# Kernel optimization log

Measured on AMD Instinct MI355X. Metric: run time of the kernel, lower is better.

The kernel has to match this reference:

```python
import jax, jax.numpy as jnp
import numpy as np

B, N, C = 32, 1024, 768
H = 12
HD = C // H            # 64
M = 2 * HD             # rand_feat_dim = head_dim * rand_feat_dim_ratio(2) = 128
LAM = 0.1
NUM_STEP = 8
EPS = 1e-12


def setup_inputs() -> dict:
    key = jax.random.key(0)
    ks = jax.random.split(key, 4)
    x = jax.random.normal(ks[0], (B, N, C), dtype=jnp.float32)
    qkv_w = jax.random.normal(ks[1], (2 * C, C), dtype=jnp.float32) * 0.02
    proj_w = jax.random.normal(ks[2], (C, C), dtype=jnp.float32) * 0.02
    proj_b = jnp.zeros((C,), dtype=jnp.float32)
    rand_matrix = jax.random.normal(ks[3], (H, HD, M), dtype=jnp.float32)
    learned_k = jnp.eye(M, dtype=jnp.float32)
    learned_lam = jnp.ones((1,), dtype=jnp.float32)
    learned_L = jnp.ones((1,), dtype=jnp.float32)
    return {"x": x, "qkv_w": qkv_w, "proj_w": proj_w, "proj_b": proj_b,
            "rand_matrix": rand_matrix, "learned_k": learned_k,
            "learned_lam": learned_lam, "learned_L": learned_L}


def _soft(z, thresh):
    # sign(z) * GELU(|z| - thresh), exact (erf) GELU as in torch nn.GELU()
    return jnp.sign(z) * jax.nn.gelu(jnp.abs(z) - thresh, approximate=False)


def reference(x, qkv_w, proj_w, proj_b, rand_matrix, learned_k, learned_lam, learned_L):
    scale = HD ** -0.5
    qkv = (x @ qkv_w.T).reshape(B, N, 2, H, HD).transpose(2, 0, 3, 1, 4)  # [2,B,H,N,HD]
    q, v = qkv[0], qkv[1]
    q = q * (scale ** 0.5)
    # performer-style positive random features: exp(x @ proj - ||x||^2/2)/sqrt(m)
    qf = jnp.exp(jnp.einsum('bhnd,hdm->bhnm', q, rand_matrix)
                 - jnp.sum(q * q, axis=-1, keepdims=True) / 2) / (M ** 0.5)
    # F.normalize(p=2, dim=-2): normalize each feature column over tokens
    qf = qf / jnp.maximum(jnp.linalg.norm(qf, axis=-2, keepdims=True), EPS)
    kk = jnp.einsum('bhnm,bhnp->bhmp', qf, qf)        # [B,H,M,M]
    inp = jnp.einsum('bhnm,bhnd->bhmd', qf, v)        # [B,H,M,HD]
    # ISTA-like sparse reconstruction
    L = jax.lax.stop_gradient(jnp.max(jnp.sum(jnp.abs(kk), axis=-1), axis=-1))[..., None, None] + 1.0
    lam_learned = learned_lam * LAM                    # broadcastable scalar
    Ll = L / learned_L                                 # [B,H,1,1]
    kk_l = jnp.einsum('mp,bhpq,qr->bhmr', learned_k, kk, learned_k)
    xs = _soft(inp, lam_learned)
    for _ in range(NUM_STEP):
        xs = xs - (jnp.einsum('bhmp,bhpd->bhmd', kk_l, xs) - inp) / Ll
        xs = _soft(xs, lam_learned / Ll)
    out = jnp.einsum('bhnm,bhmd->bhnd', qf, xs)        # [B,H,N,HD]
    out = out.transpose(0, 2, 1, 3).reshape(B, N, C)
    return out @ proj_w.T + proj_b
```

## Files before the change

kernel.cpp:

```cpp
#include <hip/hip_runtime.h>
#include <math.h>

typedef unsigned short u16;
typedef unsigned int u32;
typedef _Float16 f16;
typedef __attribute__((ext_vector_type(8))) short bf16x8;
typedef __attribute__((ext_vector_type(8))) _Float16 f16x8;
typedef __attribute__((ext_vector_type(4))) float f32x4;

constexpr int Bc = 32, Nc = 1024, Cc = 768, Hc = 12, HDc = 64, Mc = 128;
constexpr int NUM_STEP_C = 8;
constexpr float QSCALE = 0.35355339059327376f;
constexpr float INV_SQRT_M = 0.088388347648318447f;
constexpr float EPSC = 1e-12f;
constexpr int FS = 136;

__device__ __forceinline__ float softf(float z, float thr) {
  float az = fabsf(z) - thr;
  float g = 0.5f * az * (1.0f + erff(az * 0.70710678118654752f));
  return (z > 0.f) ? g : ((z < 0.f) ? -g : 0.f);
}

__device__ __forceinline__ u16 f2bf(float f) {
  u32 u = __float_as_uint(f);
  u += 0x7fffu + ((u >> 16) & 1u);
  return (u16)(u >> 16);
}

__device__ __forceinline__ f32x4 fzero() {
  f32x4 z; z[0] = 0.f; z[1] = 0.f; z[2] = 0.f; z[3] = 0.f; return z;
}

__device__ __forceinline__ f32x4 mfma16(bf16x8 a, bf16x8 b, f32x4 c) {
  return __builtin_amdgcn_mfma_f32_16x16x32_bf16(a, b, c, 0, 0, 0);
}
__device__ __forceinline__ f32x4 mfma16h(f16x8 a, f16x8 b, f32x4 c) {
  return __builtin_amdgcn_mfma_f32_16x16x32_f16(a, b, c, 0, 0, 0);
}

#define SWZ_COL(col, row) ((col) ^ (((row) & 7) << 3))

__device__ __forceinline__ void stage_swz(const u16* __restrict__ g, int ld,
                                          u16* lds, int w, int lane) {
  const int rr = lane >> 3;
  const int cs = ((lane & 7) ^ rr) << 3;
#pragma unroll
  for (int c = 0; c < 4; ++c) {
    const int r0 = w * 32 + c * 8;
    __builtin_amdgcn_global_load_lds(
        (const __attribute__((address_space(1))) void*)(g + (size_t)(r0 + rr) * ld + cs),
        (__attribute__((address_space(3))) void*)(lds + r0 * 64), 16, 0, 0);
  }
}

__global__ __launch_bounds__(256) void prep_kernel(
    const float* __restrict__ x, const float* __restrict__ qw,
    const float* __restrict__ pw, const float* __restrict__ rnd,
    const float* __restrict__ lkf, u16* __restrict__ xbf,
    u16* __restrict__ wbf, u16* __restrict__ pwbf, u16* __restrict__ randt,
    f16* __restrict__ lk16, f16* __restrict__ lkT16) {
  const int NX8 = 3145728, NW8 = 147456, NP8 = 73728, NR = 98304;
  const int NK8 = 2048, NKT = 16384;
  const int total = NX8 + NW8 + NP8 + NR + NK8 + NKT;
  for (int idx = blockIdx.x * 256 + threadIdx.x; idx < total;
       idx += gridDim.x * 256) {
    if (idx < NX8 + NW8 + NP8) {
      const float* src; u16* dst; int k;
      if (idx < NX8) { src = x; dst = xbf; k = idx; }
      else if (idx < NX8 + NW8) { src = qw; dst = wbf; k = idx - NX8; }
      else { src = pw; dst = pwbf; k = idx - NX8 - NW8; }
      float4 a = *(const float4*)(src + (size_t)k * 8);
      float4 b = *(const float4*)(src + (size_t)k * 8 + 4);
      uint4 o;
      o.x = (u32)f2bf(a.x) | ((u32)f2bf(a.y) << 16);
      o.y = (u32)f2bf(a.z) | ((u32)f2bf(a.w) << 16);
      o.z = (u32)f2bf(b.x) | ((u32)f2bf(b.y) << 16);
      o.w = (u32)f2bf(b.z) | ((u32)f2bf(b.w) << 16);
      *(uint4*)(dst + (size_t)k * 8) = o;
    } else if (idx < NX8 + NW8 + NP8 + NR) {
      int k = idx - NX8 - NW8 - NP8;
      int h = k >> 13, rem = k & 8191, m = rem >> 6, d = rem & 63;
      randt[k] = f2bf(rnd[(size_t)h * 8192 + d * 128 + m]);
    } else if (idx < NX8 + NW8 + NP8 + NR + NK8) {
      int k = idx - (NX8 + NW8 + NP8 + NR);
      float4 a = *(const float4*)(lkf + (size_t)k * 8);
      float4 b = *(const float4*)(lkf + (size_t)k * 8 + 4);
      union { f16 h[8]; uint4 u; } z;
      z.h[0] = (f16)a.x; z.h[1] = (f16)a.y; z.h[2] = (f16)a.z; z.h[3] = (f16)a.w;
      z.h[4] = (f16)b.x; z.h[5] = (f16)b.y; z.h[6] = (f16)b.z; z.h[7] = (f16)b.w;
      *(uint4*)(lk16 + (size_t)k * 8) = z.u;
    } else {
      int k = idx - (NX8 + NW8 + NP8 + NR + NK8);
      int c = k >> 7, p = k & 127;
      lkT16[k] = (f16)lkf[p * 128 + c];
    }
  }
}

__global__ __launch_bounds__(256) void qkv_qf_kernel(
    const u16* __restrict__ xbf, const u16* __restrict__ wbf,
    const u16* __restrict__ randt, u16* __restrict__ qft,
    u16* __restrict__ vbt) {
  __shared__ __align__(16) u16 SH[32768];
  const int t = threadIdx.x;
  const int hblk = blockIdx.x;
  const int lin = (hblk & 7) * 384 + (hblk >> 3);
  const int bi = lin / 12, bj = lin % 12;
  const int w = t >> 6, lane = t & 63, ln = lane & 15, kg = lane >> 4;
  const int wr = w >> 1, wc = w & 1;
  f32x4 acc[4][4];
#pragma unroll
  for (int i = 0; i < 4; ++i)
#pragma unroll
    for (int j = 0; j < 4; ++j) acc[i][j] = fzero();
  const u16* Ag = xbf + (size_t)(bi * 128) * Cc;
  const u16* Bg = wbf + (size_t)(bj * 128) * Cc;
  stage_swz(Ag, Cc, SH, w, lane);
  stage_swz(Bg, Cc, SH + 8192, w, lane);
  __syncthreads();
  int cur = 0;
  for (int tt = 0; tt < 12; ++tt) {
    if (tt < 11) {
      stage_swz(Ag + (tt + 1) * 64, Cc, SH + (cur ^ 1) * 16384, w, lane);
      stage_swz(Bg + (tt + 1) * 64, Cc, SH + 8192 + (cur ^ 1) * 16384, w, lane);
    }
    const u16* Als = SH + cur * 16384;
    const u16* Bls = SH + 8192 + cur * 16384;
#pragma unroll
    for (int ks = 0; ks < 2; ++ks) {
      const int cb = ks * 32 + kg * 8;
      bf16x8 af[4], bf[4];
#pragma unroll
      for (int i = 0; i < 4; ++i)
        af[i] = *(const bf16x8*)(Als + (wr * 64 + i * 16 + ln) * 64 +
                                 SWZ_COL(cb, ln));
#pragma unroll
      for (int j = 0; j < 4; ++j)
        bf[j] = *(const bf16x8*)(Bls + (wc * 64 + j * 16 + ln) * 64 +
                                 SWZ_COL(cb, ln));
#pragma unroll
      for (int i = 0; i < 4; ++i)
#pragma unroll
        for (int j = 0; j < 4; ++j) acc[i][j] = mfma16(af[i], bf[j], acc[i][j]);
    }
    __syncthreads();
    cur ^= 1;
  }
  const int b = bi >> 3;
  const int ntile = (bi & 7) * 128;
  if (bj >= 6) {
    const int h = (bj - 6) * 2 + wc;
    u16* vt = vbt + ((size_t)(b * Hc + h) * 64) * 1024;
#pragma unroll
    for (int i = 0; i < 4; ++i)
#pragma unroll
      for (int j = 0; j < 4; ++j) {
        int d = j * 16 + ln;
        int n0 = ntile + wr * 64 + i * 16 + kg * 4;
        uint2 pv;
        pv.x = (u32)f2bf(acc[i][j][0]) | ((u32)f2bf(acc[i][j][1]) << 16);
        pv.y = (u32)f2bf(acc[i][j][2]) | ((u32)f2bf(acc[i][j][3]) << 16);
        *(uint2*)(vt + (size_t)d * 1024 + n0) = pv;
      }
  } else {
#pragma unroll
    for (int i = 0; i < 4; ++i)
#pragma unroll
      for (int j = 0; j < 4; ++j) acc[i][j] *= QSCALE;
    float hn[4][4];
#pragma unroll
    for (int i = 0; i < 4; ++i)
#pragma unroll
      for (int r = 0; r < 4; ++r) {
        float s = acc[i][0][r] * acc[i][0][r] + acc[i][1][r] * acc[i][1][r] +
                  acc[i][2][r] * acc[i][2][r] + acc[i][3][r] * acc[i][3][r];
        s += __shfl_xor(s, 1); s += __shfl_xor(s, 2);
        s += __shfl_xor(s, 4); s += __shfl_xor(s, 8);
        hn[i][r] = 0.5f * s;
      }
    u16* Qls = SH;
#pragma unroll
    for (int i = 0; i < 4; ++i)
#pragma unroll
      for (int j = 0; j < 4; ++j)
#pragma unroll
        for (int r = 0; r < 4; ++r)
          Qls[(size_t)(wc * 128 + wr * 64 + i * 16 + kg * 4 + r) * 72 +
              j * 16 + ln] = f2bf(acc[i][j][r]);
    __syncthreads();
    const int hq = bj * 2 + (w & 1);
    const int r0q = (w >> 1) * 64;
    const u16* rt = randt + (size_t)hq * Mc * HDc;
    u16* qtb = qft + ((size_t)(b * Hc + hq) * Mc) * Nc;
    const u16* qsl = Qls + (size_t)(w & 1) * 128 * 72;
#pragma unroll
    for (int mh = 0; mh < 2; ++mh) {
      f32x4 a2[4][4];
#pragma unroll
      for (int i = 0; i < 4; ++i)
#pragma unroll
        for (int j = 0; j < 4; ++j) a2[i][j] = fzero();
#pragma unroll
      for (int ks = 0; ks < 2; ++ks) {
        bf16x8 af[4], bfr[4];
#pragma unroll
        for (int i = 0; i < 4; ++i)
          af[i] = *(const bf16x8*)(qsl + (size_t)(r0q + i * 16 + ln) * 72 +
                                   ks * 32 + kg * 8);
#pragma unroll
        for (int j = 0; j < 4; ++j)
          bfr[j] = *(const bf16x8*)(rt +
                                    (size_t)(mh * 64 + j * 16 + ln) * 64 +
                                    ks * 32 + kg * 8);
#pragma unroll
        for (int i = 0; i < 4; ++i)
#pragma unroll
          for (int j = 0; j < 4; ++j)
            a2[i][j] = mfma16(af[i], bfr[j], a2[i][j]);
      }
#pragma unroll
      for (int i = 0; i < 4; ++i)
#pragma unroll
        for (int j = 0; j < 4; ++j) {
          const int m = mh * 64 + j * 16 + ln;
          const int n0 = ntile + r0q + i * 16 + kg * 4;
          float e0 = __expf(a2[i][j][0] - hn[i][0]) * INV_SQRT_M;
          float e1 = __expf(a2[i][j][1] - hn[i][1]) * INV_SQRT_M;
          float e2 = __expf(a2[i][j][2] - hn[i][2]) * INV_SQRT_M;
          float e3 = __expf(a2[i][j][3] - hn[i][3]) * INV_SQRT_M;
          uint2 pv;
          pv.x = (u32)f2bf(e0) | ((u32)f2bf(e1) << 16);
          pv.y = (u32)f2bf(e2) | ((u32)f2bf(e3) << 16);
          *(uint2*)(qtb + (size_t)m * Nc + n0) = pv;
        }
    }
  }
}

__global__ __launch_bounds__(384) void kk_inp_kernel(
    const u16* __restrict__ qft, const u16* __restrict__ vbt,
    float* __restrict__ kk, float* __restrict__ inp) {
  __shared__ __align__(16) u16 SH[24576];
  const int t = threadIdx.x, bh = blockIdx.x;
  const int w = t >> 6, lane = t & 63, ln = lane & 15, kg = lane >> 4;
  const int wr = w / 3, wc = w % 3;
  const u16* qg = qft + (size_t)bh * Mc * Nc;
  const u16* vg = vbt + (size_t)bh * 64 * Nc;
  const int rr = lane >> 3;
  const int cs = ((lane & 7) ^ rr) << 3;
  f32x4 acc[4][4];
#pragma unroll
  for (int i = 0; i < 4; ++i)
#pragma unroll
    for (int j = 0; j < 4; ++j) acc[i][j] = fzero();

  auto stage = [&](int kt, int buf) {
    u16* Atl = SH + buf * 12288;
    u16* Vtl = Atl + 8192;
    const int n0 = kt * 64;
#pragma unroll
    for (int q = 0; q < 4; ++q) {
      const int idx = w * 4 + q;
      if (idx < 16) {
        __builtin_amdgcn_global_load_lds(
            (const __attribute__((address_space(1))) void*)(
                qg + (size_t)(idx * 8 + rr) * Nc + n0 + cs),
            (__attribute__((address_space(3))) void*)(Atl + idx * 8 * 64), 16,
            0, 0);
      } else {
        __builtin_amdgcn_global_load_lds(
            (const __attribute__((address_space(1))) void*)(
                vg + (size_t)((idx - 16) * 8 + rr) * Nc + n0 + cs),
            (__attribute__((address_space(3))) void*)(Vtl + (idx - 16) * 8 * 64),
            16, 0, 0);
      }
    }
  };

  stage(0, 0);
  __syncthreads();
  int cur = 0;
  for (int kt = 0; kt < 16; ++kt) {
    if (kt < 15) stage(kt + 1, cur ^ 1);
    const u16* Atl = SH + cur * 12288;
    const u16* Vtl = Atl + 8192;
#pragma unroll
    for (int ks = 0; ks < 2; ++ks) {
      const int cb = ks * 32 + kg * 8;
      bf16x8 af[4], bf[4];
#pragma unroll
      for (int i = 0; i < 4; ++i)
        af[i] = *(const bf16x8*)(Atl + (wr * 64 + i * 16 + ln) * 64 +
                                 SWZ_COL(cb, ln));
      if (wc < 2) {
#pragma unroll
        for (int j = 0; j < 4; ++j)
          bf[j] = *(const bf16x8*)(Atl + (wc * 64 + j * 16 + ln) * 64 +
                                   SWZ_COL(cb, ln));
      } else {
#pragma unroll
        for (int j = 0; j < 4; ++j)
          bf[j] = *(const bf16x8*)(Vtl + (j * 16 + ln) * 64 + SWZ_COL(cb, ln));
      }
#pragma unroll
      for (int i = 0; i < 4; ++i)
#pragma unroll
        for (int j = 0; j < 4; ++j) acc[i][j] = mfma16(af[i], bf[j], acc[i][j]);
    }
    __syncthreads();
    cur ^= 1;
  }
  if (wc < 2) {
    float* og = kk + (size_t)bh * Mc * Mc;
#pragma unroll
    for (int i = 0; i < 4; ++i)
#pragma unroll
      for (int j = 0; j < 4; ++j)
#pragma unroll
        for (int r = 0; r < 4; ++r)
          og[(size_t)(wr * 64 + i * 16 + kg * 4 + r) * Mc + wc * 64 + j * 16 +
             ln] = acc[i][j][r];
  } else {
    float* og = inp + (size_t)bh * Mc * HDc;
#pragma unroll
    for (int i = 0; i < 4; ++i)
#pragma unroll
      for (int j = 0; j < 4; ++j)
#pragma unroll
        for (int r = 0; r < 4; ++r)
          og[(size_t)(wr * 64 + i * 16 + kg * 4 + r) * HDc + j * 16 + ln] =
              acc[i][j][r];
  }
}

__global__ __launch_bounds__(256) void solve_kernel(
    const float* __restrict__ kk, const float* __restrict__ inp,
    const f16* __restrict__ lk16, const f16* __restrict__ lkT16,
    const float* __restrict__ lamp, const float* __restrict__ Lp,
    u16* __restrict__ xsst) {
  __shared__ __align__(16) f16 A1[128 * FS];
  __shared__ __align__(16) f16 B1[128 * FS];
  __shared__ float nrm[128], inr[128];
  __shared__ float rsum2[256];
  __shared__ float Lsh;
  const int t = threadIdx.x, bh = blockIdx.x;
  const int w = t >> 6, lane = t & 63, ln = lane & 15, kq = lane >> 4;
  const float* kkg = kk + (size_t)bh * 16384;
  if (t < 128) {
    float nm = fmaxf(sqrtf(kkg[t * 128 + t]), EPSC);
    nrm[t] = nm;
    inr[t] = 1.0f / nm;
  }
#pragma unroll
  for (int c = 0; c < 8; ++c) {
    int ch = c * 256 + t;
    int r = ch >> 4, q8 = (ch & 15) * 8;
    *(uint4*)&B1[r * FS + q8] = *(const uint4*)&lkT16[r * 128 + q8];
  }
  __syncthreads();
#pragma unroll
  for (int c = 0; c < 16; ++c) {
    int ch = c * 256 + t;
    int m = ch >> 5, p4 = (ch & 31) * 4;
    float4 v = *(const float4*)&kkg[m * 128 + p4];
    float im = inr[m];
    union { f16 h[4]; uint2 u; } z;
    z.h[0] = (f16)(v.x * im * inr[p4]);
    z.h[1] = (f16)(v.y * im * inr[p4 + 1]);
    z.h[2] = (f16)(v.z * im * inr[p4 + 2]);
    z.h[3] = (f16)(v.w * im * inr[p4 + 3]);
    *(uint2*)&A1[m * FS + p4] = z.u;
  }
  __syncthreads();
  {
    const int m = t & 127, hf = (t >> 7) * 64;
    float s = 0.f;
#pragma unroll 8
    for (int p = 0; p < 64; ++p) s += fabsf((float)A1[m * FS + hf + p]);
    rsum2[t] = s;
  }
  f32x4 t1a[2][8];
#pragma unroll
  for (int i = 0; i < 2; ++i)
#pragma unroll
    for (int j = 0; j < 8; ++j) t1a[i][j] = fzero();
  __syncthreads();
  if (t == 0) {
    float mx = 0.f;
    for (int i = 0; i < 128; ++i) mx = fmaxf(mx, rsum2[i] + rsum2[i + 128]);
    Lsh = mx + 1.0f;
  }
#pragma unroll
  for (int ks = 0; ks < 4; ++ks) {
    f16x8 a[2], b[8];
#pragma unroll
    for (int i = 0; i < 2; ++i)
      a[i] = *(const f16x8*)&A1[(w * 32 + i * 16 + ln) * FS + ks * 32 + kq * 8];
#pragma unroll
    for (int j = 0; j < 8; ++j)
      b[j] = *(const f16x8*)&B1[(j * 16 + ln) * FS + ks * 32 + kq * 8];
#pragma unroll
    for (int i = 0; i < 2; ++i)
#pragma unroll
      for (int j = 0; j < 8; ++j) t1a[i][j] = mfma16h(a[i], b[j], t1a[i][j]);
  }
  __syncthreads();
#pragma unroll
  for (int i = 0; i < 2; ++i)
#pragma unroll
    for (int j = 0; j < 8; ++j) {
      const int r = j * 16 + ln, p0 = w * 32 + i * 16 + kq * 4;
      union { f16 h[4]; uint2 u; } z;
      z.h[0] = (f16)t1a[i][j][0]; z.h[1] = (f16)t1a[i][j][1];
      z.h[2] = (f16)t1a[i][j][2]; z.h[3] = (f16)t1a[i][j][3];
      *(uint2*)&A1[r * FS + p0] = z.u;
    }
#pragma unroll
  for (int c = 0; c < 8; ++c) {
    int ch = c * 256 + t;
    int r = ch >> 4, q8 = (ch & 15) * 8;
    *(uint4*)&B1[r * FS + q8] = *(const uint4*)&lk16[r * 128 + q8];
  }
  __syncthreads();
  f32x4 kla[2][8];
#pragma unroll
  for (int i = 0; i < 2; ++i)
#pragma unroll
    for (int j = 0; j < 8; ++j) kla[i][j] = fzero();
#pragma unroll
  for (int ks = 0; ks < 4; ++ks) {
    f16x8 a[2], b[8];
#pragma unroll
    for (int i = 0; i < 2; ++i)
      a[i] = *(const f16x8*)&B1[(w * 32 + i * 16 + ln) * FS + ks * 32 + kq * 8];
#pragma unroll
    for (int j = 0; j < 8; ++j)
      b[j] = *(const f16x8*)&A1[(j * 16 + ln) * FS + ks * 32 + kq * 8];
#pragma unroll
    for (int i = 0; i < 2; ++i)
#pragma unroll
      for (int j = 0; j < 8; ++j) kla[i][j] = mfma16h(a[i], b[j], kla[i][j]);
  }
  __syncthreads();
#pragma unroll
  for (int i = 0; i < 2; ++i)
#pragma unroll
    for (int j = 0; j < 8; ++j)
#pragma unroll
      for (int r = 0; r < 4; ++r)
        B1[(w * 32 + i * 16 + kq * 4 + r) * FS + j * 16 + ln] =
            (f16)kla[i][j][r];
  const float lam = lamp[0] * 0.1f;
  const float Ll = Lsh / Lp[0];
  const float thr = lam / Ll;
  const float invLl = 1.0f / Ll;
  const float* ig = inp + (size_t)bh * 8192;
  float ri[2][4][4], xr[2][4][4];
#pragma unroll
  for (int i = 0; i < 2; ++i)
#pragma unroll
    for (int j = 0; j < 4; ++j)
#pragma unroll
      for (int r = 0; r < 4; ++r) {
        const int m = w * 32 + i * 16 + kq * 4 + r;
        const int d = j * 16 + ln;
        ri[i][j][r] = ig[m * 64 + d] * inr[m];
        xr[i][j][r] = softf(ri[i][j][r], lam);
      }
  __syncthreads();
#pragma unroll
  for (int i = 0; i < 2; ++i)
#pragma unroll
    for (int j = 0; j < 4; ++j) {
      const int d = j * 16 + ln, m0 = w * 32 + i * 16 + kq * 4;
      union { f16 h[4]; uint2 u; } z;
      z.h[0] = (f16)xr[i][j][0]; z.h[1] = (f16)xr[i][j][1];
      z.h[2] = (f16)xr[i][j][2]; z.h[3] = (f16)xr[i][j][3];
      *(uint2*)&A1[d * FS + m0] = z.u;
    }
  __syncthreads();
  for (int s = 0; s < NUM_STEP_C; ++s) {
    f32x4 acc[2][4];
#pragma unroll
    for (int i = 0; i < 2; ++i)
#pragma unroll
      for (int j = 0; j < 4; ++j) acc[i][j] = fzero();
#pragma unroll
    for (int ks = 0; ks < 4; ++ks) {
      f16x8 a[2], b[4];
#pragma unroll
      for (int i = 0; i < 2; ++i)
        a[i] = *(const f16x8*)&B1[(w * 32 + i * 16 + ln) * FS + ks * 32 + kq * 8];
#pragma unroll
      for (int j = 0; j < 4; ++j)
        b[j] = *(const f16x8*)&A1[(j * 16 + ln) * FS + ks * 32 + kq * 8];
#pragma unroll
      for (int i = 0; i < 2; ++i)
#pragma unroll
        for (int j = 0; j < 4; ++j) acc[i][j] = mfma16h(a[i], b[j], acc[i][j]);
    }
#pragma unroll
    for (int i = 0; i < 2; ++i)
#pragma unroll
      for (int j = 0; j < 4; ++j)
#pragma unroll
        for (int r = 0; r < 4; ++r)
          xr[i][j][r] =
              softf(xr[i][j][r] - (acc[i][j][r] - ri[i][j][r]) * invLl, thr);
    __syncthreads();
#pragma unroll
    for (int i = 0; i < 2; ++i)
#pragma unroll
      for (int j = 0; j < 4; ++j) {
        const int d = j * 16 + ln, m0 = w * 32 + i * 16 + kq * 4;
        union { f16 h[4]; uint2 u; } z;
        z.h[0] = (f16)xr[i][j][0]; z.h[1] = (f16)xr[i][j][1];
        z.h[2] = (f16)xr[i][j][2]; z.h[3] = (f16)xr[i][j][3];
        *(uint2*)&A1[d * FS + m0] = z.u;
      }
    __syncthreads();
  }
  u16* og = xsst + (size_t)bh * 8192;
#pragma unroll
  for (int i = 0; i < 2; ++i)
#pragma unroll
    for (int j = 0; j < 4; ++j) {
      const int d = j * 16 + ln, m0 = w * 32 + i * 16 + kq * 4;
      uint2 pv;
      pv.x = (u32)f2bf(xr[i][j][0] * inr[m0]) |
             ((u32)f2bf(xr[i][j][1] * inr[m0 + 1]) << 16);
      pv.y = (u32)f2bf(xr[i][j][2] * inr[m0 + 2]) |
             ((u32)f2bf(xr[i][j][3] * inr[m0 + 3]) << 16);
      *(uint2*)&og[d * 128 + m0] = pv;
    }
}

__global__ __launch_bounds__(256) void pvout_kernel(
    const u16* __restrict__ qft, const u16* __restrict__ xsst,
    u16* __restrict__ attn) {
  const int t = threadIdx.x;
  const int bh = blockIdx.x, nt = blockIdx.y;
  const int b = bh / Hc, h = bh % Hc;
  const int w = t >> 6, lane = t & 63, ln = lane & 15, kg = lane >> 4;
  const u16* qt = qft + (size_t)bh * Mc * Nc;
  const u16* xg = xsst + (size_t)bh * HDc * Mc;
  f32x4 acc[2][4];
#pragma unroll
  for (int i = 0; i < 2; ++i)
#pragma unroll
    for (int j = 0; j < 4; ++j) acc[i][j] = fzero();
#pragma unroll
  for (int ks = 0; ks < 4; ++ks) {
    const int m8 = ks * 32 + kg * 8;
    bf16x8 af[2];
#pragma unroll
    for (int i = 0; i < 2; ++i) {
      const int n = nt * 128 + w * 32 + i * 16 + ln;
      const u16* p = qt + (size_t)m8 * Nc + n;
#pragma unroll
      for (int e = 0; e < 8; ++e) af[i][e] = (short)p[(size_t)e * Nc];
    }
    bf16x8 bf[4];
#pragma unroll
    for (int j = 0; j < 4; ++j)
      bf[j] = *(const bf16x8*)(xg + (size_t)(j * 16 + ln) * Mc + m8);
#pragma unroll
    for (int i = 0; i < 2; ++i)
#pragma unroll
      for (int j = 0; j < 4; ++j) acc[i][j] = mfma16(af[i], bf[j], acc[i][j]);
  }
#pragma unroll
  for (int i = 0; i < 2; ++i)
#pragma unroll
    for (int j = 0; j < 4; ++j)
#pragma unroll
      for (int r = 0; r < 4; ++r) {
        int n = nt * 128 + w * 32 + i * 16 + kg * 4 + r;
        attn[((size_t)(b * Nc + n)) * Cc + h * 64 + j * 16 + ln] =
            f2bf(acc[i][j][r]);
      }
}

__global__ __launch_bounds__(256) void proj_kernel(
    const u16* __restrict__ abf, const u16* __restrict__ pwbf,
    const float* __restrict__ bias, float* __restrict__ out) {
  __shared__ __align__(16) u16 SH[32768];
  const int t = threadIdx.x;
  const int hblk = blockIdx.x;
  const int lin = (hblk & 7) * 192 + (hblk >> 3);
  const int bi = lin / 6, bj = lin % 6;
  const int w = t >> 6, lane = t & 63, ln = lane & 15, kg = lane >> 4;
  const int wr = w >> 1, wc = w & 1;
  f32x4 acc[4][4];
#pragma unroll
  for (int i = 0; i < 4; ++i)
#pragma unroll
    for (int j = 0; j < 4; ++j) acc[i][j] = fzero();
  const u16* Ag = abf + (size_t)(bi * 128) * Cc;
  const u16* Bg = pwbf + (size_t)(bj * 128) * Cc;
  stage_swz(Ag, Cc, SH, w, lane);
  stage_swz(Bg, Cc, SH + 8192, w, lane);
  __syncthreads();
  int cur = 0;
  for (int tt = 0; tt < 12; ++tt) {
    if (tt < 11) {
      stage_swz(Ag + (tt + 1) * 64, Cc, SH + (cur ^ 1) * 16384, w, lane);
      stage_swz(Bg + (tt + 1) * 64, Cc, SH + 8192 + (cur ^ 1) * 16384, w, lane);
    }
    const u16* Als = SH + cur * 16384;
    const u16* Bls = SH + 8192 + cur * 16384;
#pragma unroll
    for (int ks = 0; ks < 2; ++ks) {
      const int cb = ks * 32 + kg * 8;
      bf16x8 af[4], bf[4];
#pragma unroll
      for (int i = 0; i < 4; ++i)
        af[i] = *(const bf16x8*)(Als + (wr * 64 + i * 16 + ln) * 64 +
                                 SWZ_COL(cb, ln));
#pragma unroll
      for (int j = 0; j < 4; ++j)
        bf[j] = *(const bf16x8*)(Bls + (wc * 64 + j * 16 + ln) * 64 +
                                 SWZ_COL(cb, ln));
#pragma unroll
      for (int i = 0; i < 4; ++i)
#pragma unroll
        for (int j = 0; j < 4; ++j) acc[i][j] = mfma16(af[i], bf[j], acc[i][j]);
    }
    __syncthreads();
    cur ^= 1;
  }
#pragma unroll
  for (int j = 0; j < 4; ++j) {
    const int gc = bj * 128 + wc * 64 + j * 16 + ln;
    const float bv = bias[gc];
#pragma unroll
    for (int i = 0; i < 4; ++i) {
      const int gr = bi * 128 + wr * 64 + i * 16 + kg * 4;
#pragma unroll
      for (int r = 0; r < 4; ++r)
        out[(size_t)(gr + r) * Cc + gc] = acc[i][j][r] + bv;
    }
  }
}

extern "C" void kernel_launch(void* const* d_in, const int* in_sizes, int n_in,
                              void* d_out, int out_size, void* d_ws,
                              size_t ws_size, hipStream_t stream) {
  const float* x = (const float*)d_in[0];
  const float* qkv_w = (const float*)d_in[1];
  const float* proj_w = (const float*)d_in[2];
  const float* proj_b = (const float*)d_in[3];
  const float* rand_matrix = (const float*)d_in[4];
  const float* learned_k = (const float*)d_in[5];
  const float* learned_lam = (const float*)d_in[6];
  const float* learned_L = (const float*)d_in[7];
  float* out = (float*)d_out;

  const size_t SX = 25165824;
  const size_t SQF = 50331648;
  const size_t SVT = 25165824;
  const size_t SXT = 3145728;
  const size_t SW = 1179648;
  const size_t SPW = 589824;
  const size_t SRT = 98304;
  const size_t SLK = 16384;
  const size_t U16TOT = SX + SQF + SVT + SXT + SW + SPW + SRT + 2 * SLK;
  const size_t SKK = 6291456, SIN = 3145728;
  const size_t need = U16TOT * 2 + (SKK + SIN) * 4;
  if (ws_size < need) return;

  u16* xbf = (u16*)d_ws;
  u16* qft = xbf + SX;
  u16* vbt = qft + SQF;
  u16* xsst = vbt + SVT;
  u16* wbf = xsst + SXT;
  u16* pwbf = wbf + SW;
  u16* randt = pwbf + SPW;
  f16* lk16 = (f16*)(randt + SRT);
  f16* lkT16 = lk16 + SLK;
  float* kkf = (float*)(lkT16 + SLK);
  float* inpf = kkf + SKK;
  u16* attnbf = xbf;

  prep_kernel<<<2048, 256, 0, stream>>>(x, qkv_w, proj_w, rand_matrix,
                                        learned_k, xbf, wbf, pwbf, randt,
                                        lk16, lkT16);
  qkv_qf_kernel<<<3072, 256, 0, stream>>>(xbf, wbf, randt, qft, vbt);
  kk_inp_kernel<<<Bc * Hc, 384, 0, stream>>>(qft, vbt, kkf, inpf);
  solve_kernel<<<Bc * Hc, 256, 0, stream>>>(kkf, inpf, lk16, lkT16,
                                            learned_lam, learned_L, xsst);
  pvout_kernel<<<dim3(Bc * Hc, Nc / 128), 256, 0, stream>>>(qft, xsst, attnbf);
  proj_kernel<<<1536, 256, 0, stream>>>(attnbf, pwbf, proj_b, out);
}
```

Before: 398.8 us.

## Single-buffer QKV/proj GEMM LDS and use fine-grained vmcnt waits in kk kernel

The QKV and projection GEMM kernels drop LDS double buffering and load each K-tile into a single buffer before computing. This halves their shared memory so more blocks can be resident per CU, but it removes the overlap of global loads with MFMA work inside a block. The kk/inp kernel replaces __syncthreads with raw s_barrier plus explicit vmcnt waits, so the next stage's loads can stay in flight while the current tile is consumed. This relies on the manual waitcnt count matching the number of outstanding loads.

```diff
diff --git a/kernel.cpp b/kernel.cpp
--- a/kernel.cpp
+++ b/kernel.cpp
@@ -14,6 +14,9 @@
 constexpr float INV_SQRT_M = 0.088388347648318447f;
 constexpr float EPSC = 1e-12f;
 constexpr int FS = 136;
+
+#define BAR_RAW() asm volatile("s_barrier" ::: "memory")
+#define WAIT_VM(N) asm volatile("s_waitcnt vmcnt(" #N ")" ::: "memory")
 
 __device__ __forceinline__ float softf(float z, float thr) {
   float az = fabsf(z) - thr;
@@ -101,7 +104,9 @@
     const u16* __restrict__ xbf, const u16* __restrict__ wbf,
     const u16* __restrict__ randt, u16* __restrict__ qft,
     u16* __restrict__ vbt) {
-  __shared__ __align__(16) u16 SH[32768];
+  __shared__ __align__(16) u16 SH[18432];
+  u16* Als = SH;
+  u16* Bls = SH + 8192;
   const int t = threadIdx.x;
   const int hblk = blockIdx.x;
   const int lin = (hblk & 7) * 384 + (hblk >> 3);
@@ -115,17 +120,10 @@
     for (int j = 0; j < 4; ++j) acc[i][j] = fzero();
   const u16* Ag = xbf + (size_t)(bi * 128) * Cc;
   const u16* Bg = wbf + (size_t)(bj * 128) * Cc;
-  stage_swz(Ag, Cc, SH, w, lane);
-  stage_swz(Bg, Cc, SH + 8192, w, lane);
-  __syncthreads();
-  int cur = 0;
-  for (int tt = 0; tt < 12; ++tt) {
-    if (tt < 11) {
-      stage_swz(Ag + (tt + 1) * 64, Cc, SH + (cur ^ 1) * 16384, w, lane);
-      stage_swz(Bg + (tt + 1) * 64, Cc, SH + 8192 + (cur ^ 1) * 16384, w, lane);
-    }
-    const u16* Als = SH + cur * 16384;
-    const u16* Bls = SH + 8192 + cur * 16384;
+  for (int k0 = 0; k0 < Cc; k0 += 64) {
+    stage_swz(Ag + k0, Cc, Als, w, lane);
+    stage_swz(Bg + k0, Cc, Bls, w, lane);
+    __syncthreads();
 #pragma unroll
     for (int ks = 0; ks < 2; ++ks) {
       const int cb = ks * 32 + kg * 8;
@@ -144,7 +142,6 @@
         for (int j = 0; j < 4; ++j) acc[i][j] = mfma16(af[i], bf[j], acc[i][j]);
     }
     __syncthreads();
-    cur ^= 1;
   }
   const int b = bi >> 3;
   const int ntile = (bi & 7) * 128;
@@ -278,10 +275,15 @@
   };
 
   stage(0, 0);
-  __syncthreads();
   int cur = 0;
   for (int kt = 0; kt < 16; ++kt) {
-    if (kt < 15) stage(kt + 1, cur ^ 1);
+    if (kt < 15) {
+      stage(kt + 1, cur ^ 1);
+      WAIT_VM(4);
+    } else {
+      WAIT_VM(0);
+    }
+    BAR_RAW();
     const u16* Atl = SH + cur * 12288;
     const u16* Vtl = Atl + 8192;
 #pragma unroll
@@ -307,7 +309,7 @@
 #pragma unroll
         for (int j = 0; j < 4; ++j) acc[i][j] = mfma16(af[i], bf[j], acc[i][j]);
     }
-    __syncthreads();
+    BAR_RAW();
     cur ^= 1;
   }
   if (wc < 2) {
@@ -584,7 +586,9 @@
 __global__ __launch_bounds__(256) void proj_kernel(
     const u16* __restrict__ abf, const u16* __restrict__ pwbf,
     const float* __restrict__ bias, float* __restrict__ out) {
-  __shared__ __align__(16) u16 SH[32768];
+  __shared__ __align__(16) u16 SH[16384];
+  u16* Als = SH;
+  u16* Bls = SH + 8192;
   const int t = threadIdx.x;
   const int hblk = blockIdx.x;
   const int lin = (hblk & 7) * 192 + (hblk >> 3);
@@ -598,17 +602,10 @@
     for (int j = 0; j < 4; ++j) acc[i][j] = fzero();
   const u16* Ag = abf + (size_t)(bi * 128) * Cc;
   const u16* Bg = pwbf + (size_t)(bj * 128) * Cc;
-  stage_swz(Ag, Cc, SH, w, lane);
-  stage_swz(Bg, Cc, SH + 8192, w, lane);
-  __syncthreads();
-  int cur = 0;
-  for (int tt = 0; tt < 12; ++tt) {
-    if (tt < 11) {
-      stage_swz(Ag + (tt + 1) * 64, Cc, SH + (cur ^ 1) * 16384, w, lane);
-      stage_swz(Bg + (tt + 1) * 64, Cc, SH + 8192 + (cur ^ 1) * 16384, w, lane);
-    }
-    const u16* Als = SH + cur * 16384;
-    const u16* Bls = SH + 8192 + cur * 16384;
+  for (int k0 = 0; k0 < Cc; k0 += 64) {
+    stage_swz(Ag + k0, Cc, Als, w, lane);
+    stage_swz(Bg + k0, Cc, Bls, w, lane);
+    __syncthreads();
 #pragma unroll
     for (int ks = 0; ks < 2; ++ks) {
       const int cb = ks * 32 + kg * 8;
@@ -627,7 +624,6 @@
         for (int j = 0; j < 4; ++j) acc[i][j] = mfma16(af[i], bf[j], acc[i][j]);
     }
     __syncthreads();
-    cur ^= 1;
   }
 #pragma unroll
   for (int j = 0; j < 4; ++j) {
```

After: 441.6 us. 1.11x slower.

## Fuse output projection qf·xs into the solve kernel via shared memory

Applied to the files above, without the earlier changes.

The separate pvout kernel is removed. The solve kernel now writes the scaled bf16 xs into shared memory and loops over all 8 token tiles, computing qf·xs with MFMA and writing the attention output directly. This drops the xs global round trip and one kernel launch. The cost is that pvout parallelism falls from 3072 blocks to 384 blocks, each doing 8 serial tiles, which may leave the GPU underutilized and make the solve kernel longer.

```diff
diff --git a/kernel.cpp b/kernel.cpp
--- a/kernel.cpp
+++ b/kernel.cpp
@@ -337,7 +337,7 @@
     const float* __restrict__ kk, const float* __restrict__ inp,
     const f16* __restrict__ lk16, const f16* __restrict__ lkT16,
     const float* __restrict__ lamp, const float* __restrict__ Lp,
-    u16* __restrict__ xsst) {
+    const u16* __restrict__ qft, u16* __restrict__ attn) {
   __shared__ __align__(16) f16 A1[128 * FS];
   __shared__ __align__(16) f16 B1[128 * FS];
   __shared__ float nrm[128], inr[128];
@@ -520,7 +520,7 @@
       }
     __syncthreads();
   }
-  u16* og = xsst + (size_t)bh * 8192;
+  u16* A1u = (u16*)A1;
 #pragma unroll
   for (int i = 0; i < 2; ++i)
 #pragma unroll
@@ -531,54 +531,49 @@
              ((u32)f2bf(xr[i][j][1] * inr[m0 + 1]) << 16);
       pv.y = (u32)f2bf(xr[i][j][2] * inr[m0 + 2]) |
              ((u32)f2bf(xr[i][j][3] * inr[m0 + 3]) << 16);
-      *(uint2*)&og[d * 128 + m0] = pv;
-    }
-}
-
-__global__ __launch_bounds__(256) void pvout_kernel(
-    const u16* __restrict__ qft, const u16* __restrict__ xsst,
-    u16* __restrict__ attn) {
-  const int t = threadIdx.x;
-  const int bh = blockIdx.x, nt = blockIdx.y;
+      *(uint2*)&A1u[d * FS + m0] = pv;
+    }
+  __syncthreads();
+  const u16* qt = qft + (size_t)bh * Mc * Nc;
   const int b = bh / Hc, h = bh % Hc;
-  const int w = t >> 6, lane = t & 63, ln = lane & 15, kg = lane >> 4;
-  const u16* qt = qft + (size_t)bh * Mc * Nc;
-  const u16* xg = xsst + (size_t)bh * HDc * Mc;
-  f32x4 acc[2][4];
-#pragma unroll
-  for (int i = 0; i < 2; ++i)
-#pragma unroll
-    for (int j = 0; j < 4; ++j) acc[i][j] = fzero();
-#pragma unroll
-  for (int ks = 0; ks < 4; ++ks) {
-    const int m8 = ks * 32 + kg * 8;
-    bf16x8 af[2];
-#pragma unroll
-    for (int i = 0; i < 2; ++i) {
-      const int n = nt * 128 + w * 32 + i * 16 + ln;
-      const u16* p = qt + (size_t)m8 * Nc + n;
-#pragma unroll
-      for (int e = 0; e < 8; ++e) af[i][e] = (short)p[(size_t)e * Nc];
-    }
-    bf16x8 bf[4];
-#pragma unroll
-    for (int j = 0; j < 4; ++j)
-      bf[j] = *(const bf16x8*)(xg + (size_t)(j * 16 + ln) * Mc + m8);
-#pragma unroll
-    for (int i = 0; i < 2; ++i)
-#pragma unroll
-      for (int j = 0; j < 4; ++j) acc[i][j] = mfma16(af[i], bf[j], acc[i][j]);
-  }
-#pragma unroll
-  for (int i = 0; i < 2; ++i)
-#pragma unroll
-    for (int j = 0; j < 4; ++j)
-#pragma unroll
-      for (int r = 0; r < 4; ++r) {
-        int n = nt * 128 + w * 32 + i * 16 + kg * 4 + r;
-        attn[((size_t)(b * Nc + n)) * Cc + h * 64 + j * 16 + ln] =
-            f2bf(acc[i][j][r]);
-      }
+  for (int nt = 0; nt < 8; ++nt) {
+    f32x4 pacc[2][4];
+#pragma unroll
+    for (int i = 0; i < 2; ++i)
+#pragma unroll
+      for (int j = 0; j < 4; ++j) pacc[i][j] = fzero();
+#pragma unroll
+    for (int ks = 0; ks < 4; ++ks) {
+      const int m8 = ks * 32 + kq * 8;
+      bf16x8 af[2];
+#pragma unroll
+      for (int i = 0; i < 2; ++i) {
+        const int n = nt * 128 + w * 32 + i * 16 + ln;
+        const u16* p = qt + (size_t)m8 * Nc + n;
+#pragma unroll
+        for (int e = 0; e < 8; ++e) af[i][e] = (short)p[(size_t)e * Nc];
+      }
+      bf16x8 bf[4];
+#pragma unroll
+      for (int j = 0; j < 4; ++j)
+        bf[j] = *(const bf16x8*)&A1u[(j * 16 + ln) * FS + m8];
+#pragma unroll
+      for (int i = 0; i < 2; ++i)
+#pragma unroll
+        for (int j = 0; j < 4; ++j)
+          pacc[i][j] = mfma16(af[i], bf[j], pacc[i][j]);
+    }
+#pragma unroll
+    for (int i = 0; i < 2; ++i)
+#pragma unroll
+      for (int j = 0; j < 4; ++j)
+#pragma unroll
+        for (int r = 0; r < 4; ++r) {
+          int n = nt * 128 + w * 32 + i * 16 + kq * 4 + r;
+          attn[((size_t)(b * Nc + n)) * Cc + h * 64 + j * 16 + ln] =
+              f2bf(pacc[i][j][r]);
+        }
+  }
 }
 
 __global__ __launch_bounds__(256) void proj_kernel(
@@ -659,12 +654,11 @@
   const size_t SX = 25165824;
   const size_t SQF = 50331648;
   const size_t SVT = 25165824;
-  const size_t SXT = 3145728;
   const size_t SW = 1179648;
   const size_t SPW = 589824;
   const size_t SRT = 98304;
   const size_t SLK = 16384;
-  const size_t U16TOT = SX + SQF + SVT + SXT + SW + SPW + SRT + 2 * SLK;
+  const size_t U16TOT = SX + SQF + SVT + SW + SPW + SRT + 2 * SLK;
   const size_t SKK = 6291456, SIN = 3145728;
   const size_t need = U16TOT * 2 + (SKK + SIN) * 4;
   if (ws_size < need) return;
@@ -672,8 +666,7 @@
   u16* xbf = (u16*)d_ws;
   u16* qft = xbf + SX;
   u16* vbt = qft + SQF;
-  u16* xsst = vbt + SVT;
-  u16* wbf = xsst + SXT;
+  u16* wbf = vbt + SVT;
   u16* pwbf = wbf + SW;
   u16* randt = pwbf + SPW;
   f16* lk16 = (f16*)(randt + SRT);
@@ -688,7 +681,7 @@
   qkv_qf_kernel<<<3072, 256, 0, stream>>>(xbf, wbf, randt, qft, vbt);
   kk_inp_kernel<<<Bc * Hc, 384, 0, stream>>>(qft, vbt, kkf, inpf);
   solve_kernel<<<Bc * Hc, 256, 0, stream>>>(kkf, inpf, lk16, lkT16,
-                                            learned_lam, learned_L, xsst);
-  pvout_kernel<<<dim3(Bc * Hc, Nc / 128), 256, 0, stream>>>(qft, xsst, attnbf);
+                                            learned_lam, learned_L, qft,
+                                            attnbf);
   proj_kernel<<<1536, 256, 0, stream>>>(attnbf, pwbf, proj_b, out);
 }
```

New measurement: 380.7 us (median of 3 runs). 4.5% less time.
